# Kernel optimization log

Hardware: AMD Instinct MI355X
Metric: run time of the kernel (lower is better)

Reference implementation:

```python
import jax, jax.numpy as jnp
import numpy as np

N, E = 20000, 320000
IN_DIM, CODE_DIM, HIDDEN, HEADS, NREL = 896, 768, 256, 4, 5
CH = HIDDEN // HEADS
CODE_WEIGHT = 3.0
NEG_SLOPE = 0.2


def _gat_layer(h, src, dst, W, att_src, att_dst, bias):
    # h: [N, HIDDEN]; src/dst already include self-loops. Eval mode -> no dropout.
    n = h.shape[0]
    x = (h @ W).reshape(n, HEADS, CH)                      # [N,H,C]
    a_src = (x * att_src).sum(-1)                          # [N,H]
    a_dst = (x * att_dst).sum(-1)                          # [N,H]
    alpha = jax.nn.leaky_relu(a_src[src] + a_dst[dst], NEG_SLOPE)  # [E',H]
    amax = jax.ops.segment_max(alpha, dst, num_segments=n)
    amax = jnp.where(jnp.isfinite(amax), amax, 0.0)
    ex = jnp.exp(alpha - amax[dst])
    denom = jax.ops.segment_sum(ex, dst, num_segments=n)
    coef = ex / denom[dst]                                 # segment softmax over in-neighbors
    msg = x[src] * coef[:, :, None]                        # [E',H,C]
    out = jax.ops.segment_sum(msg, dst, num_segments=n)    # [N,H,C]
    return out.reshape(n, HEADS * CH) + bias


def setup_inputs() -> dict:
    key = jax.random.key(0)
    ks = jax.random.split(key, 20)
    def glorot(k, shape):
        fan_in = shape[0]
        return jax.random.normal(k, shape, jnp.float32) / jnp.sqrt(jnp.asarray(fan_in, jnp.float32))
    inp = {
        "x": jax.random.normal(ks[0], (N, IN_DIM), jnp.float32),
        "edge_index": jax.random.randint(ks[1], (2, E), 0, N, jnp.int32),
        "edge_type": jax.random.randint(ks[2], (E,), 0, NREL, jnp.int32),
        "edge_weight": jax.random.uniform(ks[3], (E,), jnp.float32),
        "rel_emb": jax.random.normal(ks[4], (NREL, HIDDEN), jnp.float32),
        "Wp": glorot(ks[5], (IN_DIM, HIDDEN)),
        "bp": jnp.zeros((HIDDEN,), jnp.float32),
        "W1": glorot(ks[6], (HIDDEN, HIDDEN)),
        "att_src1": glorot(ks[7], (HEADS, CH)) * 0.1,
        "att_dst1": glorot(ks[8], (HEADS, CH)) * 0.1,
        "b1": jnp.zeros((HIDDEN,), jnp.float32),
        "W2": glorot(ks[9], (HIDDEN, HIDDEN)),
        "att_src2": glorot(ks[10], (HEADS, CH)) * 0.1,
        "att_dst2": glorot(ks[11], (HEADS, CH)) * 0.1,
        "b2": jnp.zeros((HIDDEN,), jnp.float32),
        "Wo": glorot(ks[12], (HIDDEN, 1)),
        "bo": jnp.zeros((1,), jnp.float32),
    }
    return inp


def reference(x, edge_index, edge_type, edge_weight, rel_emb, Wp, bp,
              W1, att_src1, att_dst1, b1, W2, att_src2, att_dst2, b2, Wo, bo):
    # feature reorder + code reweighting
    x_code = x[:, :CODE_DIM]
    x_num = x[:, CODE_DIM:]
    xc = jnp.concatenate([x_num, CODE_WEIGHT * x_code], axis=-1)
    h = jax.nn.relu(xc @ Wp + bp)                          # [N,HIDDEN]

    src, dst = edge_index[0], edge_index[1]
    # relational message + index_add scatter
    rel = rel_emb[edge_type] * edge_weight[:, None]        # [E,HIDDEN]
    msg = h[src] + rel
    h = h + jax.ops.segment_sum(msg, dst, num_segments=N)

    # GATConv adds self-loops by default
    loop = jnp.arange(N, dtype=src.dtype)
    src_sl = jnp.concatenate([src, loop])
    dst_sl = jnp.concatenate([dst, loop])

    h = _gat_layer(h, src_sl, dst_sl, W1, att_src1, att_dst1, b1)
    h = _gat_layer(h, src_sl, dst_sl, W2, att_src2, att_dst2, b2)
    score = (h @ Wo + bo)[:, 0]                            # [N]
    return score
```

## Files before the change

kernel.cpp:

```cpp
#include <hip/hip_runtime.h>
#include <hip/hip_bf16.h>

#define N_NODES 20000
#define E_EDGES 320000

typedef __attribute__((ext_vector_type(8))) short s8v;
typedef __attribute__((ext_vector_type(4))) float f4v;

__device__ __forceinline__ float lrelu(float v){ return v > 0.f ? v : 0.2f * v; }

__device__ __forceinline__ float bitf(unsigned short u){
  union { unsigned int i; float f; } v; v.i = ((unsigned int)u) << 16; return v.f;
}
__device__ __forceinline__ float4 bf4(const unsigned short* p){
  ushort4 u = *(const ushort4*)p;
  return make_float4(bitf(u.x), bitf(u.y), bitf(u.z), bitf(u.w));
}
__device__ __forceinline__ unsigned short bfhi(float v){
  union{float f; unsigned u;} a; a.f = v;
  unsigned r = a.u + 0x7FFFu + ((a.u >> 16) & 1u);
  return (unsigned short)(r >> 16);
}
__device__ __forceinline__ float bf2f(unsigned short h){
  union{unsigned u; float f;} a; a.u = ((unsigned)h) << 16; return a.f;
}
__device__ __forceinline__ void split2(float v0, float v1, unsigned& hu, unsigned& lu){
  __hip_bfloat162 h2 = __float22bfloat162_rn(make_float2(v0, v1));
  unsigned h; __builtin_memcpy(&h, &h2, 4);
  union{unsigned u; float f;} c0, c1;
  c0.u = h << 16;
  c1.u = h & 0xFFFF0000u;
  __hip_bfloat162 l2 = __float22bfloat162_rn(make_float2(v0 - c0.f, v1 - c1.f));
  unsigned l; __builtin_memcpy(&l, &l2, 4);
  hu = h; lu = l;
}

__global__ __launch_bounds__(256) void k_count(const int* __restrict__ dst, int* __restrict__ deg, int E){
  int e = blockIdx.x * 256 + threadIdx.x;
  if (e < E) atomicAdd(&deg[dst[e]], 1);
}

__global__ __launch_bounds__(256) void k_scan(const int* __restrict__ deg, int* __restrict__ off,
                                              int* __restrict__ cur, int n){
  __shared__ int part[256];
  __shared__ int base[257];
  int tid = threadIdx.x;
  int chunk = (n + 255) / 256;
  int st = tid * chunk;
  int en = st + chunk; if (en > n) en = n;
  int s = 0;
  for (int i = st; i < en; ++i) s += deg[i];
  part[tid] = s;
  __syncthreads();
  if (tid == 0){
    int a = 0;
    for (int i = 0; i < 256; ++i){ base[i] = a; a += part[i]; }
    base[256] = a;
  }
  __syncthreads();
  int a = base[tid];
  for (int i = st; i < en; ++i){ off[i] = a; cur[i] = 0; a += deg[i]; }
  if (tid == 0) off[n] = base[256];
}

__global__ __launch_bounds__(256) void k_fill(const int* __restrict__ src, const int* __restrict__ dst,
                       const int* __restrict__ ety, const float* __restrict__ ew,
                       const int* __restrict__ off, int* __restrict__ cur,
                       int* __restrict__ csrc, int* __restrict__ cet, float* __restrict__ cw, int E){
  int e = blockIdx.x * 256 + threadIdx.x;
  if (e < E){
    int d = dst[e];
    int p = atomicAdd(&cur[d], 1);
    int i = off[d] + p;
    csrc[i] = src[e];
    cet[i]  = ety[e];
    cw[i]   = ew[e];
  }
}

__global__ __launch_bounds__(64) void k_prep(const float* __restrict__ W, unsigned short* __restrict__ Bp, int K){
  int kt = blockIdx.x;
  int n  = blockIdx.y * 64 + threadIdx.x;
  unsigned short hi[32], lo[32];
#pragma unroll
  for (int kk = 0; kk < 32; ++kk){
    float v = W[(size_t)(kt * 32 + kk) * 256 + n];
    unsigned short h = bfhi(v);
    hi[kk] = h;
    lo[kk] = bfhi(v - bf2f(h));
  }
  size_t plane = (size_t)(K >> 5) * 256 * 32;
  size_t b = ((size_t)kt * 256 + n) * 32;
#pragma unroll
  for (int kk = 0; kk < 32; ++kk){
    Bp[b + kk]         = hi[kk];
    Bp[plane + b + kk] = lo[kk];
  }
}

template<int KT, bool PERM, bool EPI, bool ATT, bool CBF>
__global__ __launch_bounds__(256) void k_mm(
    const float* __restrict__ A, const unsigned short* __restrict__ Bp,
    const float* __restrict__ bias, void* __restrict__ Cout,
    const float* __restrict__ attS, const float* __restrict__ attD,
    float* __restrict__ aS, float* __restrict__ aD, int M)
{
  constexpr int K = KT * 32;
  __shared__ unsigned short Ah[64 * 40];
  __shared__ unsigned short Al[64 * 40];

  const int tid  = threadIdx.x;
  const int lane = tid & 63;
  const int w    = tid >> 6;
  const int wm   = w >> 1;
  const int wn   = w & 1;
  const int l15  = lane & 15;
  const int kg   = lane >> 4;
  const int m0   = blockIdx.x * 64;
  const int n0   = blockIdx.y * 128;
  const size_t planeB = (size_t)KT * 256 * 32;

  f4v acc[2][4];
#pragma unroll
  for (int f = 0; f < 2; ++f)
#pragma unroll
    for (int g = 0; g < 4; ++g)
#pragma unroll
      for (int r = 0; r < 4; ++r) acc[f][g][r] = 0.f;

  const int arow = tid >> 2;
  const int aj   = tid & 3;
  const int gr   = m0 + arow;

  auto loadA = [&](float* v, int kt){
    if (gr < M){
      if constexpr (PERM){
        int c = kt * 32 + aj * 8;
        const float* sp; float sc;
        if (c < 128){ sp = A + (size_t)gr * 896 + (768 + c); sc = 1.f; }
        else        { sp = A + (size_t)gr * 896 + (c - 128); sc = 3.f; }
        float4 f0 = *(const float4*)sp;
        float4 f1 = *(const float4*)(sp + 4);
        v[0]=f0.x*sc; v[1]=f0.y*sc; v[2]=f0.z*sc; v[3]=f0.w*sc;
        v[4]=f1.x*sc; v[5]=f1.y*sc; v[6]=f1.z*sc; v[7]=f1.w*sc;
      } else {
        const float* sp = A + (size_t)gr * K + kt * 32 + aj * 8;
        float4 f0 = *(const float4*)sp;
        float4 f1 = *(const float4*)(sp + 4);
        v[0]=f0.x; v[1]=f0.y; v[2]=f0.z; v[3]=f0.w;
        v[4]=f1.x; v[5]=f1.y; v[6]=f1.z; v[7]=f1.w;
      }
    } else {
#pragma unroll
      for (int j = 0; j < 8; ++j) v[j] = 0.f;
    }
  };

  float av[8];
  loadA(av, 0);

  for (int kt = 0; kt < KT; ++kt){
    {
      union { unsigned u[4]; s8v s; } hv, lv;
#pragma unroll
      for (int p = 0; p < 4; ++p)
        split2(av[2*p], av[2*p+1], hv.u[p], lv.u[p]);
      *(s8v*)&Ah[arow * 40 + aj * 8] = hv.s;
      *(s8v*)&Al[arow * 40 + aj * 8] = lv.s;
    }
    __syncthreads();
    float nv[8];
    if (kt + 1 < KT) loadA(nv, kt + 1);
    s8v bh[4], bl[4];
#pragma unroll
    for (int g = 0; g < 4; ++g){
      const unsigned short* bp2 = Bp + ((size_t)kt * 256 + n0 + wn * 64 + g * 16 + l15) * 32 + kg * 8;
      bh[g] = *(const s8v*)bp2;
      bl[g] = *(const s8v*)(bp2 + planeB);
    }
    s8v ah[2], al[2];
#pragma unroll
    for (int f = 0; f < 2; ++f){
      int row = wm * 32 + f * 16 + l15;
      ah[f] = *(const s8v*)&Ah[row * 40 + kg * 8];
      al[f] = *(const s8v*)&Al[row * 40 + kg * 8];
    }
#pragma unroll
    for (int f = 0; f < 2; ++f)
#pragma unroll
      for (int g = 0; g < 4; ++g){
        acc[f][g] = __builtin_amdgcn_mfma_f32_16x16x32_bf16(ah[f], bh[g], acc[f][g], 0, 0, 0);
        acc[f][g] = __builtin_amdgcn_mfma_f32_16x16x32_bf16(ah[f], bl[g], acc[f][g], 0, 0, 0);
        acc[f][g] = __builtin_amdgcn_mfma_f32_16x16x32_bf16(al[f], bh[g], acc[f][g], 0, 0, 0);
      }
    __syncthreads();
    if (kt + 1 < KT){
#pragma unroll
      for (int j = 0; j < 8; ++j) av[j] = nv[j];
    }
  }

#pragma unroll
  for (int f = 0; f < 2; ++f){
#pragma unroll
    for (int g = 0; g < 4; ++g){
      int col = n0 + wn * 64 + g * 16 + l15;
      float bb = EPI ? bias[col] : 0.f;
#pragma unroll
      for (int r = 0; r < 4; ++r){
        int row = m0 + wm * 32 + f * 16 + kg * 4 + r;
        if (row < M){
          float v = acc[f][g][r];
          if constexpr (EPI) v = fmaxf(v + bb, 0.f);
          if constexpr (CBF) ((unsigned short*)Cout)[(size_t)row * 256 + col] = bfhi(v);
          else               ((float*)Cout)[(size_t)row * 256 + col] = v;
        }
      }
    }
  }

  if constexpr (ATT){
    const int head = (n0 >> 6) + wn;
    float sv[4], dv[4];
#pragma unroll
    for (int g = 0; g < 4; ++g){
      int col = n0 + wn * 64 + g * 16 + l15;
      sv[g] = attS[col];
      dv[g] = attD[col];
    }
#pragma unroll
    for (int f = 0; f < 2; ++f){
#pragma unroll
      for (int r = 0; r < 4; ++r){
        float ps = acc[f][0][r]*sv[0] + acc[f][1][r]*sv[1] + acc[f][2][r]*sv[2] + acc[f][3][r]*sv[3];
        float pd = acc[f][0][r]*dv[0] + acc[f][1][r]*dv[1] + acc[f][2][r]*dv[2] + acc[f][3][r]*dv[3];
#pragma unroll
        for (int mm = 1; mm < 16; mm <<= 1){
          ps += __shfl_xor(ps, mm, 64);
          pd += __shfl_xor(pd, mm, 64);
        }
        int row = m0 + wm * 32 + f * 16 + kg * 4 + r;
        if (l15 == 0 && row < M){
          aS[(size_t)row * 4 + head] = ps;
          aD[(size_t)row * 4 + head] = pd;
        }
      }
    }
  }
}

__global__ __launch_bounds__(256) void k_agg(
    const unsigned short* __restrict__ h0, const int* __restrict__ off,
    const int* __restrict__ csrc, const int* __restrict__ cet, const float* __restrict__ cw,
    const float* __restrict__ rel, float* __restrict__ h1, int N)
{
  int n = blockIdx.x * 4 + (threadIdx.x >> 6);
  if (n >= N) return;
  int lane = threadIdx.x & 63;
  int c0 = lane * 4;
  float4 acc = bf4(&h0[(size_t)n * 256 + c0]);
  int s0 = off[n], s1 = off[n + 1];
  int e = s0;
  for (; e + 3 < s1; e += 4){
    int sA = csrc[e], sB = csrc[e+1], sC = csrc[e+2], sD = csrc[e+3];
    int tA = cet[e],  tB = cet[e+1],  tC = cet[e+2],  tD = cet[e+3];
    float wA = cw[e], wB = cw[e+1], wC = cw[e+2], wD = cw[e+3];
    float4 hA = bf4(&h0[(size_t)sA * 256 + c0]);
    float4 hB = bf4(&h0[(size_t)sB * 256 + c0]);
    float4 hC = bf4(&h0[(size_t)sC * 256 + c0]);
    float4 hD = bf4(&h0[(size_t)sD * 256 + c0]);
    float4 rA = *(const float4*)&rel[(size_t)tA * 256 + c0];
    float4 rB = *(const float4*)&rel[(size_t)tB * 256 + c0];
    float4 rC = *(const float4*)&rel[(size_t)tC * 256 + c0];
    float4 rD = *(const float4*)&rel[(size_t)tD * 256 + c0];
    acc.x += hA.x + hB.x + hC.x + hD.x + rA.x*wA + rB.x*wB + rC.x*wC + rD.x*wD;
    acc.y += hA.y + hB.y + hC.y + hD.y + rA.y*wA + rB.y*wB + rC.y*wC + rD.y*wD;
    acc.z += hA.z + hB.z + hC.z + hD.z + rA.z*wA + rB.z*wB + rC.z*wC + rD.z*wD;
    acc.w += hA.w + hB.w + hC.w + hD.w + rA.w*wA + rB.w*wB + rC.w*wC + rD.w*wD;
  }
  for (; e < s1; ++e){
    int s = csrc[e];
    int t = cet[e];
    float wg = cw[e];
    float4 hv = bf4(&h0[(size_t)s * 256 + c0]);
    float4 rv = *(const float4*)&rel[(size_t)t * 256 + c0];
    acc.x += hv.x + rv.x * wg;
    acc.y += hv.y + rv.y * wg;
    acc.z += hv.z + rv.z * wg;
    acc.w += hv.w + rv.w * wg;
  }
  *(float4*)&h1[(size_t)n * 256 + c0] = acc;
}

template<bool SCORE>
__global__ __launch_bounds__(256) void k_gat(
    const unsigned short* __restrict__ xh, const float* __restrict__ aS, const float* __restrict__ aD,
    const int* __restrict__ off, const int* __restrict__ csrc,
    const float* __restrict__ bias, float* __restrict__ hout,
    const float* __restrict__ Wo, const float* __restrict__ bo, float* __restrict__ out, int N)
{
  int n = blockIdx.x * 4 + (threadIdx.x >> 6);
  if (n >= N) return;
  int lane = threadIdx.x & 63;
  int head = lane >> 4;
  int c0 = lane * 4;
  int s0 = off[n], s1 = off[n + 1];

  float ad0, ad1, ad2, ad3;
  { float4 t = *(const float4*)&aD[(size_t)n * 4]; ad0 = t.x; ad1 = t.y; ad2 = t.z; ad3 = t.w; }
  float q0, q1, q2, q3;
  { float4 t = *(const float4*)&aS[(size_t)n * 4];
    q0 = lrelu(t.x + ad0); q1 = lrelu(t.y + ad1); q2 = lrelu(t.z + ad2); q3 = lrelu(t.w + ad3); }

  for (int base = s0; base < s1; base += 64){
    int e = base + lane;
    if (e < s1){
      int s = csrc[e];
      float4 av = *(const float4*)&aS[(size_t)s * 4];
      q0 = fmaxf(q0, lrelu(av.x + ad0));
      q1 = fmaxf(q1, lrelu(av.y + ad1));
      q2 = fmaxf(q2, lrelu(av.z + ad2));
      q3 = fmaxf(q3, lrelu(av.w + ad3));
    }
  }
#pragma unroll
  for (int mm = 1; mm < 64; mm <<= 1){
    q0 = fmaxf(q0, __shfl_xor(q0, mm, 64));
    q1 = fmaxf(q1, __shfl_xor(q1, mm, 64));
    q2 = fmaxf(q2, __shfl_xor(q2, mm, 64));
    q3 = fmaxf(q3, __shfl_xor(q3, mm, 64));
  }
  float adh = head == 0 ? ad0 : (head == 1 ? ad1 : (head == 2 ? ad2 : ad3));
  float mh  = head == 0 ? q0  : (head == 1 ? q1  : (head == 2 ? q2  : q3));

  float ash = aS[(size_t)n * 4 + head];
  float ex = __expf(lrelu(ash + adh) - mh);
  float den = ex;
  float4 xv = bf4(&xh[(size_t)n * 256 + c0]);
  float4 acc;
  acc.x = ex * xv.x; acc.y = ex * xv.y; acc.z = ex * xv.z; acc.w = ex * xv.w;

  int e = s0;
  for (; e + 3 < s1; e += 4){
    int sA = csrc[e], sB = csrc[e+1], sC = csrc[e+2], sD = csrc[e+3];
    float aA = aS[(size_t)sA * 4 + head];
    float aB = aS[(size_t)sB * 4 + head];
    float aC = aS[(size_t)sC * 4 + head];
    float aD2 = aS[(size_t)sD * 4 + head];
    float4 xA = bf4(&xh[(size_t)sA * 256 + c0]);
    float4 xB = bf4(&xh[(size_t)sB * 256 + c0]);
    float4 xC = bf4(&xh[(size_t)sC * 256 + c0]);
    float4 xD = bf4(&xh[(size_t)sD * 256 + c0]);
    float eA = __expf(lrelu(aA + adh) - mh);
    float eB = __expf(lrelu(aB + adh) - mh);
    float eC = __expf(lrelu(aC + adh) - mh);
    float eD = __expf(lrelu(aD2 + adh) - mh);
    den += eA + eB + eC + eD;
    acc.x = fmaf(eA, xA.x, fmaf(eB, xB.x, fmaf(eC, xC.x, fmaf(eD, xD.x, acc.x))));
    acc.y = fmaf(eA, xA.y, fmaf(eB, xB.y, fmaf(eC, xC.y, fmaf(eD, xD.y, acc.y))));
    acc.z = fmaf(eA, xA.z, fmaf(eB, xB.z, fmaf(eC, xC.z, fmaf(eD, xD.z, acc.z))));
    acc.w = fmaf(eA, xA.w, fmaf(eB, xB.w, fmaf(eC, xC.w, fmaf(eD, xD.w, acc.w))));
  }
  for (; e < s1; ++e){
    int s = csrc[e];
    float a  = aS[(size_t)s * 4 + head];
    float e2 = __expf(lrelu(a + adh) - mh);
    den += e2;
    float4 x2 = bf4(&xh[(size_t)s * 256 + c0]);
    acc.x = fmaf(e2, x2.x, acc.x);
    acc.y = fmaf(e2, x2.y, acc.y);
    acc.z = fmaf(e2, x2.z, acc.z);
    acc.w = fmaf(e2, x2.w, acc.w);
  }
  float inv = 1.f / den;
  float4 bb = *(const float4*)&bias[c0];
  float4 o;
  o.x = acc.x * inv + bb.x;
  o.y = acc.y * inv + bb.y;
  o.z = acc.z * inv + bb.z;
  o.w = acc.w * inv + bb.w;
  if constexpr (SCORE){
    float4 wv = *(const float4*)&Wo[c0];
    float p = o.x * wv.x + o.y * wv.y + o.z * wv.z + o.w * wv.w;
#pragma unroll
    for (int mm = 1; mm < 64; mm <<= 1) p += __shfl_xor(p, mm, 64);
    if (lane == 0) out[n] = p + bo[0];
  } else {
    *(float4*)&hout[(size_t)n * 256 + c0] = o;
  }
}

extern "C" void kernel_launch(void* const* d_in, const int* in_sizes, int n_in,
                              void* d_out, int out_size, void* d_ws, size_t ws_size,
                              hipStream_t stream)
{
  const float* x   = (const float*)d_in[0];
  const int*   ei  = (const int*)  d_in[1];
  const int*   ety = (const int*)  d_in[2];
  const float* ew  = (const float*)d_in[3];
  const float* rel = (const float*)d_in[4];
  const float* Wp  = (const float*)d_in[5];
  const float* bp  = (const float*)d_in[6];
  const float* W1  = (const float*)d_in[7];
  const float* as1 = (const float*)d_in[8];
  const float* ad1 = (const float*)d_in[9];
  const float* b1  = (const float*)d_in[10];
  const float* W2  = (const float*)d_in[11];
  const float* as2 = (const float*)d_in[12];
  const float* ad2 = (const float*)d_in[13];
  const float* b2  = (const float*)d_in[14];
  const float* Wo  = (const float*)d_in[15];
  const float* bo  = (const float*)d_in[16];
  float* out = (float*)d_out;

  const int N = N_NODES, E = E_EDGES;
  char* w = (char*)d_ws;
  size_t o = 0;
  auto alloc = [&](size_t bytes) -> char* {
    char* p = w + o;
    o = (o + bytes + 255) & ~(size_t)255;
    return p;
  };
  unsigned short* h0b = (unsigned short*)alloc((size_t)N * 256 * 2);
  unsigned short* xhb = (unsigned short*)alloc((size_t)N * 256 * 2);
  float* h1  = (float*)alloc((size_t)N * 256 * 4);
  float* aS  = (float*)alloc((size_t)N * 4 * 4);
  float* aD  = (float*)alloc((size_t)N * 4 * 4);
  int* deg   = (int*)alloc((size_t)N * 4);
  int* offs  = (int*)alloc((size_t)(N + 1) * 4);
  int* cur   = (int*)alloc((size_t)N * 4);
  int* csrc  = (int*)alloc((size_t)E * 4);
  int* cet   = (int*)alloc((size_t)E * 4);
  float* cw  = (float*)alloc((size_t)E * 4);
  unsigned short* BpP = (unsigned short*)alloc((size_t)2 * 896 * 256 * 2);
  unsigned short* Bp1 = (unsigned short*)alloc((size_t)2 * 256 * 256 * 2);
  unsigned short* Bp2 = (unsigned short*)alloc((size_t)2 * 256 * 256 * 2);

  const int* srcp = ei;
  const int* dstp = ei + E;

  hipMemsetAsync(deg, 0, (size_t)N * 4, stream);
  k_count<<<(E + 255) / 256, 256, 0, stream>>>(dstp, deg, E);
  k_scan<<<1, 256, 0, stream>>>(deg, offs, cur, N);
  k_fill<<<(E + 255) / 256, 256, 0, stream>>>(srcp, dstp, ety, ew, offs, cur, csrc, cet, cw, E);

  k_prep<<<dim3(896 / 32, 4), 64, 0, stream>>>(Wp, BpP, 896);
  k_prep<<<dim3(256 / 32, 4), 64, 0, stream>>>(W1, Bp1, 256);
  k_prep<<<dim3(256 / 32, 4), 64, 0, stream>>>(W2, Bp2, 256);

  dim3 ggrid((N + 63) / 64, 2);
  int nblk = (N + 3) / 4;

  k_mm<28, true, true, false, true><<<ggrid, 256, 0, stream>>>(
      x, BpP, bp, (void*)h0b, nullptr, nullptr, nullptr, nullptr, N);
  k_agg<<<nblk, 256, 0, stream>>>(h0b, offs, csrc, cet, cw, rel, h1, N);
  k_mm<8, false, false, true, true><<<ggrid, 256, 0, stream>>>(
      h1, Bp1, nullptr, (void*)xhb, as1, ad1, aS, aD, N);
  k_gat<false><<<nblk, 256, 0, stream>>>(xhb, aS, aD, offs, csrc, b1, h1, nullptr, nullptr, nullptr, N);
  k_mm<8, false, false, true, true><<<ggrid, 256, 0, stream>>>(
      h1, Bp2, nullptr, (void*)xhb, as2, ad2, aS, aD, N);
  k_gat<true><<<nblk, 256, 0, stream>>>(xhb, aS, aD, offs, csrc, b2, nullptr, Wo, bo, out, N);
}
```

Measured before the change: 289.9 us.

## Double-buffer LDS in GEMM, shrink N-tile to 64, flatten grid with M-major block order

The split-bf16 MFMA GEMM now double-buffers the A tile in LDS and prefetches B fragments one k-step ahead, dropping one barrier per iteration. The N tile shrinks from 128 to 64 columns so each block covers one attention head, and attention-logit partials from the two wave columns are combined through shared memory. Blocks are launched on a 1D grid with the four N-tiles of a row adjacent, and launch bounds request 4 blocks per CU. In exchange, A rows are loaded and split four times instead of twice, which means more redundant A traffic, especially in the 896-wide projection.

```diff
diff --git a/kernel.cpp b/kernel.cpp
--- a/kernel.cpp
+++ b/kernel.cpp
@@ -99,15 +99,17 @@
 }
 
 template<int KT, bool PERM, bool EPI, bool ATT, bool CBF>
-__global__ __launch_bounds__(256) void k_mm(
+__global__ __launch_bounds__(256, 4) void k_mm(
     const float* __restrict__ A, const unsigned short* __restrict__ Bp,
     const float* __restrict__ bias, void* __restrict__ Cout,
     const float* __restrict__ attS, const float* __restrict__ attD,
     float* __restrict__ aS, float* __restrict__ aD, int M)
 {
   constexpr int K = KT * 32;
-  __shared__ unsigned short Ah[64 * 40];
-  __shared__ unsigned short Al[64 * 40];
+  __shared__ unsigned short AhB[2][64 * 40];
+  __shared__ unsigned short AlB[2][64 * 40];
+  __shared__ float smS[2][2][4][4][2];
+  __shared__ float smD[2][2][4][4][2];
 
   const int tid  = threadIdx.x;
   const int lane = tid & 63;
@@ -116,15 +118,17 @@
   const int wn   = w & 1;
   const int l15  = lane & 15;
   const int kg   = lane >> 4;
-  const int m0   = blockIdx.x * 64;
-  const int n0   = blockIdx.y * 128;
+  const int bid  = blockIdx.x;
+  const int m0   = (bid >> 2) * 64;
+  const int by   = bid & 3;
+  const int n0   = by * 64;
   const size_t planeB = (size_t)KT * 256 * 32;
 
-  f4v acc[2][4];
+  f4v acc[2][2];
 #pragma unroll
   for (int f = 0; f < 2; ++f)
 #pragma unroll
-    for (int g = 0; g < 4; ++g)
+    for (int g = 0; g < 2; ++g)
 #pragma unroll
       for (int r = 0; r < 4; ++r) acc[f][g][r] = 0.f;
 
@@ -155,56 +159,64 @@
       for (int j = 0; j < 8; ++j) v[j] = 0.f;
     }
   };
+  auto writeLDS = [&](const float* v, int buf){
+    union { unsigned u[4]; s8v s; } hv, lv;
+#pragma unroll
+    for (int p = 0; p < 4; ++p)
+      split2(v[2*p], v[2*p+1], hv.u[p], lv.u[p]);
+    *(s8v*)&AhB[buf][arow * 40 + aj * 8] = hv.s;
+    *(s8v*)&AlB[buf][arow * 40 + aj * 8] = lv.s;
+  };
+  auto loadB = [&](s8v* bh, s8v* bl, int kt){
+#pragma unroll
+    for (int g = 0; g < 2; ++g){
+      const unsigned short* bp2 = Bp + ((size_t)kt * 256 + n0 + wn * 32 + g * 16 + l15) * 32 + kg * 8;
+      bh[g] = *(const s8v*)bp2;
+      bl[g] = *(const s8v*)(bp2 + planeB);
+    }
+  };
 
   float av[8];
   loadA(av, 0);
-
+  writeLDS(av, 0);
+  if (KT > 1) loadA(av, 1);
+  s8v bh[2], bl[2];
+  loadB(bh, bl, 0);
+
+  int cur = 0;
   for (int kt = 0; kt < KT; ++kt){
-    {
-      union { unsigned u[4]; s8v s; } hv, lv;
-#pragma unroll
-      for (int p = 0; p < 4; ++p)
-        split2(av[2*p], av[2*p+1], hv.u[p], lv.u[p]);
-      *(s8v*)&Ah[arow * 40 + aj * 8] = hv.s;
-      *(s8v*)&Al[arow * 40 + aj * 8] = lv.s;
-    }
     __syncthreads();
-    float nv[8];
-    if (kt + 1 < KT) loadA(nv, kt + 1);
-    s8v bh[4], bl[4];
-#pragma unroll
-    for (int g = 0; g < 4; ++g){
-      const unsigned short* bp2 = Bp + ((size_t)kt * 256 + n0 + wn * 64 + g * 16 + l15) * 32 + kg * 8;
-      bh[g] = *(const s8v*)bp2;
-      bl[g] = *(const s8v*)(bp2 + planeB);
-    }
+    if (kt + 1 < KT) writeLDS(av, cur ^ 1);
+    if (kt + 2 < KT) loadA(av, kt + 2);
+    s8v nbh[2], nbl[2];
+    if (kt + 1 < KT) loadB(nbh, nbl, kt + 1);
     s8v ah[2], al[2];
 #pragma unroll
     for (int f = 0; f < 2; ++f){
       int row = wm * 32 + f * 16 + l15;
-      ah[f] = *(const s8v*)&Ah[row * 40 + kg * 8];
-      al[f] = *(const s8v*)&Al[row * 40 + kg * 8];
+      ah[f] = *(const s8v*)&AhB[cur][row * 40 + kg * 8];
+      al[f] = *(const s8v*)&AlB[cur][row * 40 + kg * 8];
     }
 #pragma unroll
     for (int f = 0; f < 2; ++f)
 #pragma unroll
-      for (int g = 0; g < 4; ++g){
+      for (int g = 0; g < 2; ++g){
         acc[f][g] = __builtin_amdgcn_mfma_f32_16x16x32_bf16(ah[f], bh[g], acc[f][g], 0, 0, 0);
         acc[f][g] = __builtin_amdgcn_mfma_f32_16x16x32_bf16(ah[f], bl[g], acc[f][g], 0, 0, 0);
         acc[f][g] = __builtin_amdgcn_mfma_f32_16x16x32_bf16(al[f], bh[g], acc[f][g], 0, 0, 0);
       }
-    __syncthreads();
     if (kt + 1 < KT){
-#pragma unroll
-      for (int j = 0; j < 8; ++j) av[j] = nv[j];
-    }
+      bh[0] = nbh[0]; bh[1] = nbh[1];
+      bl[0] = nbl[0]; bl[1] = nbl[1];
+    }
+    cur ^= 1;
   }
 
 #pragma unroll
   for (int f = 0; f < 2; ++f){
 #pragma unroll
-    for (int g = 0; g < 4; ++g){
-      int col = n0 + wn * 64 + g * 16 + l15;
+    for (int g = 0; g < 2; ++g){
+      int col = n0 + wn * 32 + g * 16 + l15;
       float bb = EPI ? bias[col] : 0.f;
 #pragma unroll
       for (int r = 0; r < 4; ++r){
@@ -220,11 +232,10 @@
   }
 
   if constexpr (ATT){
-    const int head = (n0 >> 6) + wn;
-    float sv[4], dv[4];
-#pragma unroll
-    for (int g = 0; g < 4; ++g){
-      int col = n0 + wn * 64 + g * 16 + l15;
+    float sv[2], dv[2];
+#pragma unroll
+    for (int g = 0; g < 2; ++g){
+      int col = n0 + wn * 32 + g * 16 + l15;
       sv[g] = attS[col];
       dv[g] = attD[col];
     }
@@ -232,18 +243,28 @@
     for (int f = 0; f < 2; ++f){
 #pragma unroll
       for (int r = 0; r < 4; ++r){
-        float ps = acc[f][0][r]*sv[0] + acc[f][1][r]*sv[1] + acc[f][2][r]*sv[2] + acc[f][3][r]*sv[3];
-        float pd = acc[f][0][r]*dv[0] + acc[f][1][r]*dv[1] + acc[f][2][r]*dv[2] + acc[f][3][r]*dv[3];
+        float ps = acc[f][0][r]*sv[0] + acc[f][1][r]*sv[1];
+        float pd = acc[f][0][r]*dv[0] + acc[f][1][r]*dv[1];
 #pragma unroll
         for (int mm = 1; mm < 16; mm <<= 1){
           ps += __shfl_xor(ps, mm, 64);
           pd += __shfl_xor(pd, mm, 64);
         }
-        int row = m0 + wm * 32 + f * 16 + kg * 4 + r;
-        if (l15 == 0 && row < M){
-          aS[(size_t)row * 4 + head] = ps;
-          aD[(size_t)row * 4 + head] = pd;
+        if (l15 == 0){
+          smS[wm][f][kg][r][wn] = ps;
+          smD[wm][f][kg][r][wn] = pd;
         }
+      }
+    }
+    __syncthreads();
+    if (tid < 64){
+      int wm2 = tid >> 5, f2 = (tid >> 4) & 1, kg2 = (tid >> 2) & 3, r2 = tid & 3;
+      int row = m0 + wm2 * 32 + f2 * 16 + kg2 * 4 + r2;
+      if (row < M){
+        float s = smS[wm2][f2][kg2][r2][0] + smS[wm2][f2][kg2][r2][1];
+        float d = smD[wm2][f2][kg2][r2][0] + smD[wm2][f2][kg2][r2][1];
+        aS[(size_t)row * 4 + by] = s;
+        aD[(size_t)row * 4 + by] = d;
       }
     }
   }
@@ -448,16 +469,16 @@
   k_prep<<<dim3(256 / 32, 4), 64, 0, stream>>>(W1, Bp1, 256);
   k_prep<<<dim3(256 / 32, 4), 64, 0, stream>>>(W2, Bp2, 256);
 
-  dim3 ggrid((N + 63) / 64, 2);
+  int gblk = ((N + 63) / 64) * 4;
   int nblk = (N + 3) / 4;
 
-  k_mm<28, true, true, false, true><<<ggrid, 256, 0, stream>>>(
+  k_mm<28, true, true, false, true><<<gblk, 256, 0, stream>>>(
       x, BpP, bp, (void*)h0b, nullptr, nullptr, nullptr, nullptr, N);
   k_agg<<<nblk, 256, 0, stream>>>(h0b, offs, csrc, cet, cw, rel, h1, N);
-  k_mm<8, false, false, true, true><<<ggrid, 256, 0, stream>>>(
+  k_mm<8, false, false, true, true><<<gblk, 256, 0, stream>>>(
       h1, Bp1, nullptr, (void*)xhb, as1, ad1, aS, aD, N);
   k_gat<false><<<nblk, 256, 0, stream>>>(xhb, aS, aD, offs, csrc, b1, h1, nullptr, nullptr, nullptr, N);
-  k_mm<8, false, false, true, true><<<ggrid, 256, 0, stream>>>(
+  k_mm<8, false, false, true, true><<<gblk, 256, 0, stream>>>(
       h1, Bp2, nullptr, (void*)xhb, as2, ad2, aS, aD, N);
   k_gat<true><<<nblk, 256, 0, stream>>>(xhb, aS, aD, offs, csrc, b2, nullptr, Wo, bo, out, N);
 }
```

After: 285.6 us. No clear change (-1.5%).

## Double-buffer GEMM A tiles in smaller blocks; cache GAT edge logits in LDS

Applied to the files above, without the earlier changes.

The GEMM kernel moves to 32-row, 128-thread blocks with double-buffered LDS A tiles. This drops one barrier per k-step and prefetches A two steps ahead. The GAT kernel computes leaky-relu logits once during the max pass, stores them with source indices in per-wave LDS (up to 128 edges), and turns them into exponentials plus denominators in a parallel pass. This avoids re-gathering aS and re-running exp per edge in the serial accumulation loop, at the cost of more LDS use and a slow fallback path for nodes with more than 128 edges.

```diff
diff --git a/kernel.cpp b/kernel.cpp
--- a/kernel.cpp
+++ b/kernel.cpp
@@ -99,24 +99,22 @@
 }
 
 template<int KT, bool PERM, bool EPI, bool ATT, bool CBF>
-__global__ __launch_bounds__(256) void k_mm(
+__global__ __launch_bounds__(128, 4) void k_mm(
     const float* __restrict__ A, const unsigned short* __restrict__ Bp,
     const float* __restrict__ bias, void* __restrict__ Cout,
     const float* __restrict__ attS, const float* __restrict__ attD,
     float* __restrict__ aS, float* __restrict__ aD, int M)
 {
   constexpr int K = KT * 32;
-  __shared__ unsigned short Ah[64 * 40];
-  __shared__ unsigned short Al[64 * 40];
+  __shared__ unsigned short AhB[2][32 * 40];
+  __shared__ unsigned short AlB[2][32 * 40];
 
   const int tid  = threadIdx.x;
   const int lane = tid & 63;
-  const int w    = tid >> 6;
-  const int wm   = w >> 1;
-  const int wn   = w & 1;
+  const int wn   = tid >> 6;
   const int l15  = lane & 15;
   const int kg   = lane >> 4;
-  const int m0   = blockIdx.x * 64;
+  const int m0   = blockIdx.x * 32;
   const int n0   = blockIdx.y * 128;
   const size_t planeB = (size_t)KT * 256 * 32;
 
@@ -155,22 +153,25 @@
       for (int j = 0; j < 8; ++j) v[j] = 0.f;
     }
   };
+  auto writeLDS = [&](const float* v, int buf){
+    union { unsigned u[4]; s8v s; } hv, lv;
+#pragma unroll
+    for (int p = 0; p < 4; ++p)
+      split2(v[2*p], v[2*p+1], hv.u[p], lv.u[p]);
+    *(s8v*)&AhB[buf][arow * 40 + aj * 8] = hv.s;
+    *(s8v*)&AlB[buf][arow * 40 + aj * 8] = lv.s;
+  };
 
   float av[8];
   loadA(av, 0);
-
+  writeLDS(av, 0);
+  if (KT > 1) loadA(av, 1);
+
+  int cur = 0;
   for (int kt = 0; kt < KT; ++kt){
-    {
-      union { unsigned u[4]; s8v s; } hv, lv;
-#pragma unroll
-      for (int p = 0; p < 4; ++p)
-        split2(av[2*p], av[2*p+1], hv.u[p], lv.u[p]);
-      *(s8v*)&Ah[arow * 40 + aj * 8] = hv.s;
-      *(s8v*)&Al[arow * 40 + aj * 8] = lv.s;
-    }
     __syncthreads();
-    float nv[8];
-    if (kt + 1 < KT) loadA(nv, kt + 1);
+    if (kt + 1 < KT) writeLDS(av, cur ^ 1);
+    if (kt + 2 < KT) loadA(av, kt + 2);
     s8v bh[4], bl[4];
 #pragma unroll
     for (int g = 0; g < 4; ++g){
@@ -181,9 +182,9 @@
     s8v ah[2], al[2];
 #pragma unroll
     for (int f = 0; f < 2; ++f){
-      int row = wm * 32 + f * 16 + l15;
-      ah[f] = *(const s8v*)&Ah[row * 40 + kg * 8];
-      al[f] = *(const s8v*)&Al[row * 40 + kg * 8];
+      int row = f * 16 + l15;
+      ah[f] = *(const s8v*)&AhB[cur][row * 40 + kg * 8];
+      al[f] = *(const s8v*)&AlB[cur][row * 40 + kg * 8];
     }
 #pragma unroll
     for (int f = 0; f < 2; ++f)
@@ -193,11 +194,7 @@
         acc[f][g] = __builtin_amdgcn_mfma_f32_16x16x32_bf16(ah[f], bl[g], acc[f][g], 0, 0, 0);
         acc[f][g] = __builtin_amdgcn_mfma_f32_16x16x32_bf16(al[f], bh[g], acc[f][g], 0, 0, 0);
       }
-    __syncthreads();
-    if (kt + 1 < KT){
-#pragma unroll
-      for (int j = 0; j < 8; ++j) av[j] = nv[j];
-    }
+    cur ^= 1;
   }
 
 #pragma unroll
@@ -208,7 +205,7 @@
       float bb = EPI ? bias[col] : 0.f;
 #pragma unroll
       for (int r = 0; r < 4; ++r){
-        int row = m0 + wm * 32 + f * 16 + kg * 4 + r;
+        int row = m0 + f * 16 + kg * 4 + r;
         if (row < M){
           float v = acc[f][g][r];
           if constexpr (EPI) v = fmaxf(v + bb, 0.f);
@@ -220,7 +217,7 @@
   }
 
   if constexpr (ATT){
-    const int head = (n0 >> 6) + wn;
+    const int head = blockIdx.y * 2 + wn;
     float sv[4], dv[4];
 #pragma unroll
     for (int g = 0; g < 4; ++g){
@@ -239,7 +236,7 @@
           ps += __shfl_xor(ps, mm, 64);
           pd += __shfl_xor(pd, mm, 64);
         }
-        int row = m0 + wm * 32 + f * 16 + kg * 4 + r;
+        int row = m0 + f * 16 + kg * 4 + r;
         if (l15 == 0 && row < M){
           aS[(size_t)row * 4 + head] = ps;
           aD[(size_t)row * 4 + head] = pd;
@@ -299,79 +296,114 @@
     const float* __restrict__ bias, float* __restrict__ hout,
     const float* __restrict__ Wo, const float* __restrict__ bo, float* __restrict__ out, int N)
 {
-  int n = blockIdx.x * 4 + (threadIdx.x >> 6);
+  __shared__ float4 exs[4][128];
+  __shared__ int   srcs[4][128];
+  const int wv   = threadIdx.x >> 6;
+  const int n    = blockIdx.x * 4 + wv;
   if (n >= N) return;
-  int lane = threadIdx.x & 63;
-  int head = lane >> 4;
-  int c0 = lane * 4;
-  int s0 = off[n], s1 = off[n + 1];
-
-  float ad0, ad1, ad2, ad3;
-  { float4 t = *(const float4*)&aD[(size_t)n * 4]; ad0 = t.x; ad1 = t.y; ad2 = t.z; ad3 = t.w; }
-  float q0, q1, q2, q3;
-  { float4 t = *(const float4*)&aS[(size_t)n * 4];
-    q0 = lrelu(t.x + ad0); q1 = lrelu(t.y + ad1); q2 = lrelu(t.z + ad2); q3 = lrelu(t.w + ad3); }
-
-  for (int base = s0; base < s1; base += 64){
-    int e = base + lane;
-    if (e < s1){
-      int s = csrc[e];
+  const int lane = threadIdx.x & 63;
+  const int head = lane >> 4;
+  const int c0   = lane * 4;
+  const int s0 = off[n], s1 = off[n + 1];
+  const int deg = s1 - s0;
+  const int nc = deg < 128 ? deg : 128;
+
+  float4 ad4 = *(const float4*)&aD[(size_t)n * 4];
+  float4 asf = *(const float4*)&aS[(size_t)n * 4];
+  float4 aself;
+  aself.x = lrelu(asf.x + ad4.x); aself.y = lrelu(asf.y + ad4.y);
+  aself.z = lrelu(asf.z + ad4.z); aself.w = lrelu(asf.w + ad4.w);
+  float4 q = aself;
+
+  for (int base = 0; base < deg; base += 64){
+    int ci = base + lane;
+    if (ci < deg){
+      int s = csrc[s0 + ci];
       float4 av = *(const float4*)&aS[(size_t)s * 4];
-      q0 = fmaxf(q0, lrelu(av.x + ad0));
-      q1 = fmaxf(q1, lrelu(av.y + ad1));
-      q2 = fmaxf(q2, lrelu(av.z + ad2));
-      q3 = fmaxf(q3, lrelu(av.w + ad3));
+      float4 al4;
+      al4.x = lrelu(av.x + ad4.x); al4.y = lrelu(av.y + ad4.y);
+      al4.z = lrelu(av.z + ad4.z); al4.w = lrelu(av.w + ad4.w);
+      q.x = fmaxf(q.x, al4.x); q.y = fmaxf(q.y, al4.y);
+      q.z = fmaxf(q.z, al4.z); q.w = fmaxf(q.w, al4.w);
+      if (ci < 128){ srcs[wv][ci] = s; exs[wv][ci] = al4; }
     }
   }
 #pragma unroll
   for (int mm = 1; mm < 64; mm <<= 1){
-    q0 = fmaxf(q0, __shfl_xor(q0, mm, 64));
-    q1 = fmaxf(q1, __shfl_xor(q1, mm, 64));
-    q2 = fmaxf(q2, __shfl_xor(q2, mm, 64));
-    q3 = fmaxf(q3, __shfl_xor(q3, mm, 64));
-  }
-  float adh = head == 0 ? ad0 : (head == 1 ? ad1 : (head == 2 ? ad2 : ad3));
-  float mh  = head == 0 ? q0  : (head == 1 ? q1  : (head == 2 ? q2  : q3));
-
-  float ash = aS[(size_t)n * 4 + head];
-  float ex = __expf(lrelu(ash + adh) - mh);
-  float den = ex;
+    q.x = fmaxf(q.x, __shfl_xor(q.x, mm, 64));
+    q.y = fmaxf(q.y, __shfl_xor(q.y, mm, 64));
+    q.z = fmaxf(q.z, __shfl_xor(q.z, mm, 64));
+    q.w = fmaxf(q.w, __shfl_xor(q.w, mm, 64));
+  }
+  asm volatile("s_waitcnt lgkmcnt(0)" ::: "memory");
+
+  float4 den4 = make_float4(0.f, 0.f, 0.f, 0.f);
+  for (int ci = lane; ci < nc; ci += 64){
+    float4 a = exs[wv][ci];
+    float4 e4;
+    e4.x = __expf(a.x - q.x); e4.y = __expf(a.y - q.y);
+    e4.z = __expf(a.z - q.z); e4.w = __expf(a.w - q.w);
+    exs[wv][ci] = e4;
+    den4.x += e4.x; den4.y += e4.y; den4.z += e4.z; den4.w += e4.w;
+  }
+#pragma unroll
+  for (int mm = 1; mm < 64; mm <<= 1){
+    den4.x += __shfl_xor(den4.x, mm, 64);
+    den4.y += __shfl_xor(den4.y, mm, 64);
+    den4.z += __shfl_xor(den4.z, mm, 64);
+    den4.w += __shfl_xor(den4.w, mm, 64);
+  }
+  asm volatile("s_waitcnt lgkmcnt(0)" ::: "memory");
+
+  const float mh  = head == 0 ? q.x : (head == 1 ? q.y : (head == 2 ? q.z : q.w));
+  const float adh = head == 0 ? ad4.x : (head == 1 ? ad4.y : (head == 2 ? ad4.z : ad4.w));
+  const float aselfh = head == 0 ? aself.x : (head == 1 ? aself.y : (head == 2 ? aself.z : aself.w));
+  float den = (head == 0 ? den4.x : (head == 1 ? den4.y : (head == 2 ? den4.z : den4.w)));
+  float exself = __expf(aselfh - mh);
+  den += exself;
+
   float4 xv = bf4(&xh[(size_t)n * 256 + c0]);
   float4 acc;
-  acc.x = ex * xv.x; acc.y = ex * xv.y; acc.z = ex * xv.z; acc.w = ex * xv.w;
-
-  int e = s0;
-  for (; e + 3 < s1; e += 4){
-    int sA = csrc[e], sB = csrc[e+1], sC = csrc[e+2], sD = csrc[e+3];
-    float aA = aS[(size_t)sA * 4 + head];
-    float aB = aS[(size_t)sB * 4 + head];
-    float aC = aS[(size_t)sC * 4 + head];
-    float aD2 = aS[(size_t)sD * 4 + head];
+  acc.x = exself * xv.x; acc.y = exself * xv.y; acc.z = exself * xv.z; acc.w = exself * xv.w;
+
+  const float* exw = (const float*)&exs[wv][0];
+  int e = 0;
+  for (; e + 3 < nc; e += 4){
+    int sA = srcs[wv][e], sB = srcs[wv][e+1], sC = srcs[wv][e+2], sD = srcs[wv][e+3];
+    float eA = exw[(e  ) * 4 + head];
+    float eB = exw[(e+1) * 4 + head];
+    float eC = exw[(e+2) * 4 + head];
+    float eD = exw[(e+3) * 4 + head];
     float4 xA = bf4(&xh[(size_t)sA * 256 + c0]);
     float4 xB = bf4(&xh[(size_t)sB * 256 + c0]);
     float4 xC = bf4(&xh[(size_t)sC * 256 + c0]);
     float4 xD = bf4(&xh[(size_t)sD * 256 + c0]);
-    float eA = __expf(lrelu(aA + adh) - mh);
-    float eB = __expf(lrelu(aB + adh) - mh);
-    float eC = __expf(lrelu(aC + adh) - mh);
-    float eD = __expf(lrelu(aD2 + adh) - mh);
-    den += eA + eB + eC + eD;
     acc.x = fmaf(eA, xA.x, fmaf(eB, xB.x, fmaf(eC, xC.x, fmaf(eD, xD.x, acc.x))));
     acc.y = fmaf(eA, xA.y, fmaf(eB, xB.y, fmaf(eC, xC.y, fmaf(eD, xD.y, acc.y))));
     acc.z = fmaf(eA, xA.z, fmaf(eB, xB.z, fmaf(eC, xC.z, fmaf(eD, xD.z, acc.z))));
     acc.w = fmaf(eA, xA.w, fmaf(eB, xB.w, fmaf(eC, xC.w, fmaf(eD, xD.w, acc.w))));
   }
-  for (; e < s1; ++e){
-    int s = csrc[e];
+  for (; e < nc; ++e){
+    int s = srcs[wv][e];
+    float ef = exw[e * 4 + head];
+    float4 x2 = bf4(&xh[(size_t)s * 256 + c0]);
+    acc.x = fmaf(ef, x2.x, acc.x);
+    acc.y = fmaf(ef, x2.y, acc.y);
+    acc.z = fmaf(ef, x2.z, acc.z);
+    acc.w = fmaf(ef, x2.w, acc.w);
+  }
+  for (int ci = 128; ci < deg; ++ci){
+    int s = csrc[s0 + ci];
     float a  = aS[(size_t)s * 4 + head];
-    float e2 = __expf(lrelu(a + adh) - mh);
-    den += e2;
+    float ef = __expf(lrelu(a + adh) - mh);
+    den += ef;
     float4 x2 = bf4(&xh[(size_t)s * 256 + c0]);
-    acc.x = fmaf(e2, x2.x, acc.x);
-    acc.y = fmaf(e2, x2.y, acc.y);
-    acc.z = fmaf(e2, x2.z, acc.z);
-    acc.w = fmaf(e2, x2.w, acc.w);
-  }
+    acc.x = fmaf(ef, x2.x, acc.x);
+    acc.y = fmaf(ef, x2.y, acc.y);
+    acc.z = fmaf(ef, x2.z, acc.z);
+    acc.w = fmaf(ef, x2.w, acc.w);
+  }
+
   float inv = 1.f / den;
   float4 bb = *(const float4*)&bias[c0];
   float4 o;
@@ -380,8 +412,8 @@
   o.z = acc.z * inv + bb.z;
   o.w = acc.w * inv + bb.w;
   if constexpr (SCORE){
-    float4 wv = *(const float4*)&Wo[c0];
-    float p = o.x * wv.x + o.y * wv.y + o.z * wv.z + o.w * wv.w;
+    float4 wvv = *(const float4*)&Wo[c0];
+    float p = o.x * wvv.x + o.y * wvv.y + o.z * wvv.z + o.w * wvv.w;
 #pragma unroll
     for (int mm = 1; mm < 64; mm <<= 1) p += __shfl_xor(p, mm, 64);
     if (lane == 0) out[n] = p + bo[0];
@@ -448,16 +480,16 @@
   k_prep<<<dim3(256 / 32, 4), 64, 0, stream>>>(W1, Bp1, 256);
   k_prep<<<dim3(256 / 32, 4), 64, 0, stream>>>(W2, Bp2, 256);
 
-  dim3 ggrid((N + 63) / 64, 2);
+  dim3 gg((N + 31) / 32, 2);
   int nblk = (N + 3) / 4;
 
-  k_mm<28, true, true, false, true><<<ggrid, 256, 0, stream>>>(
+  k_mm<28, true, true, false, true><<<gg, 128, 0, stream>>>(
       x, BpP, bp, (void*)h0b, nullptr, nullptr, nullptr, nullptr, N);
   k_agg<<<nblk, 256, 0, stream>>>(h0b, offs, csrc, cet, cw, rel, h1, N);
-  k_mm<8, false, false, true, true><<<ggrid, 256, 0, stream>>>(
+  k_mm<8, false, false, true, true><<<gg, 128, 0, stream>>>(
       h1, Bp1, nullptr, (void*)xhb, as1, ad1, aS, aD, N);
   k_gat<false><<<nblk, 256, 0, stream>>>(xhb, aS, aD, offs, csrc, b1, h1, nullptr, nullptr, nullptr, N);
-  k_mm<8, false, false, true, true><<<ggrid, 256, 0, stream>>>(
+  k_mm<8, false, false, true, true><<<gg, 128, 0, stream>>>(
       h1, Bp2, nullptr, (void*)xhb, as2, ad2, aS, aD, N);
   k_gat<true><<<nblk, 256, 0, stream>>>(xhb, aS, aD, offs, csrc, b2, nullptr, Wo, bo, out, N);
 }
```

Result: faster. 272.3 us (-6.1%).
